# Kernel tuning notes

Measured on AMD Instinct MI355X. Metric: run time of the kernel, lower is better.

Reference implementation:

```python
import jax, jax.numpy as jnp
import numpy as np


def setup_inputs() -> dict:
    key = jax.random.key(0)
    k1, k2, k3 = jax.random.split(key, 3)
    B, C, E, L, W = 4, 2, 256, 16000, 40
    mixture_w = jax.random.normal(k1, (B, E, L), dtype=jnp.float32)
    est_mask = jax.random.uniform(k2, (B, C, E, L), dtype=jnp.float32)
    basis_w = jax.random.normal(k3, (W, E), dtype=jnp.float32) * (1.0 / np.sqrt(E))
    return {"mixture_w": mixture_w, "est_mask": est_mask, "basis_w": basis_w}


def overlap_and_add(frames, frame_step):
    # frames: [B, C, L, W] -> [B, C, T] with T = (L-1)*frame_step + W
    B, C, L, W = frames.shape
    T = (L - 1) * frame_step + W
    # scatter-add each frame into the output waveform at its strided offset
    idx = (jnp.arange(L)[:, None] * frame_step + jnp.arange(W)[None, :]).reshape(-1)
    out = jnp.zeros((B, C, T), dtype=frames.dtype)
    return out.at[..., idx].add(frames.reshape(B, C, L * W))


def reference(mixture_w, est_mask, basis_w):
    # mixture_w: [B, E, L], est_mask: [B, C, E, L], basis_w: [W, E]
    source_w = mixture_w[:, None, :, :] * est_mask          # [B, C, E, L]
    # transpose(2,3) then Linear(E->W): contract over E
    est_frames = jnp.einsum('bcel,we->bclw', source_w, basis_w)  # [B, C, L, W]
    W = basis_w.shape[0]
    return overlap_and_add(est_frames, W // 2)              # [B, C, T]
```

## Files before the change

### kernel.cpp

```cpp
#include <hip/hip_runtime.h>

#define BQ   4
#define CQ   2
#define EQ   256
#define LQ   16000
#define WQ   40
#define STEP 20
#define TQ   ((LQ - 1) * STEP + WQ)
#define TLF  255
#define OWN  (TLF * STEP)
#define NBX  63
#define SPAN (TLF * STEP + WQ)

__global__ void transpose_basis_kernel(const float* __restrict__ basis,
                                       float* __restrict__ wsT) {
    int i = blockIdx.x * 256 + threadIdx.x;
    if (i < EQ * WQ) {
        int e = i / WQ;
        int w = i - e * WQ;
        wsT[i] = basis[w * EQ + e];
    }
}

__global__ __launch_bounds__(256, 4) void decoder_kernel(
    const float* __restrict__ mix,
    const float* __restrict__ mask,
    const float* __restrict__ wsT,
    float* __restrict__ out)
{
    __shared__ float outS[SPAN];

    const int tid = threadIdx.x;
    const int ll  = tid;
    const int bx  = blockIdx.x;
    const int b   = blockIdx.y;
    const int c   = blockIdx.z;
    const int f   = TLF * bx - 1 + ll;

    const int   fc    = min(max(f, 0), LQ - 1);
    const float valid = (f >= 0 && f < LQ) ? 1.0f : 0.0f;

    float acc[WQ];
#pragma unroll
    for (int w = 0; w < WQ; ++w) acc[w] = 0.0f;

    const float* mp = mix  + (size_t)b * EQ * LQ + fc;
    const float* kp = mask + ((size_t)(b * CQ + c)) * EQ * LQ + fc;

    for (int eo = 0; eo < EQ; eo += 4) {
        float m[4], k[4];
#pragma unroll
        for (int u = 0; u < 4; ++u) {
            m[u] = mp[(size_t)(eo + u) * LQ];
            k[u] = kp[(size_t)(eo + u) * LQ];
        }
#pragma unroll
        for (int u = 0; u < 4; ++u) {
            const float s  = m[u] * k[u] * valid;
            const float* bb = wsT + (eo + u) * WQ;
#pragma unroll
            for (int w = 0; w < WQ; ++w) acc[w] = fmaf(s, bb[w], acc[w]);
        }
    }

    const int base = ll * STEP;
    if ((ll & 1) == 0) {
#pragma unroll
        for (int w = 0; w < WQ; ++w) outS[base + w] = acc[w];
    }
    __syncthreads();
    if (ll & 1) {
#pragma unroll
        for (int w = 0; w < WQ; ++w) outS[base + w] += acc[w];
    }
    __syncthreads();

    const size_t ob = ((size_t)b * CQ + c) * TQ + (size_t)OWN * bx;
    for (int i = tid; i < OWN; i += 256) {
        const long t = (long)OWN * bx + i;
        if (t < (long)TQ) {
            out[ob + i] = outS[STEP + i];
        }
    }
}

extern "C" void kernel_launch(void* const* d_in, const int* in_sizes, int n_in,
                              void* d_out, int out_size, void* d_ws, size_t ws_size,
                              hipStream_t stream) {
    const float* mix   = (const float*)d_in[0];
    const float* mask  = (const float*)d_in[1];
    const float* basis = (const float*)d_in[2];
    float* out = (float*)d_out;
    float* wsT = (float*)d_ws;

    transpose_basis_kernel<<<dim3((EQ * WQ + 255) / 256), 256, 0, stream>>>(basis, wsT);

    dim3 grid(NBX, BQ, CQ);
    decoder_kernel<<<grid, 256, 0, stream>>>(mix, mask, wsT, out);
}
```

Before: 283.4 us.

## Split E reduction across waves, stage basis in LDS, four frames per thread

Each of the four waves in a block now reduces over its own quarter of the E dimension instead of each thread walking all 256. Each lane accumulates four frames in float4 registers, and the basis is staged once into shared memory and read back as broadcast float4 values. The four per-wave partial results are combined through two shared overlap-add buffers in four serialized phases, and the two buffers are summed at write-out. The goal is more independent loads in flight and a shorter serial dependency chain per thread, at the cost of higher register use (launch bounds lowered to 2), larger LDS use and extra barriers.

```diff
diff --git a/kernel.cpp b/kernel.cpp
--- a/kernel.cpp
+++ b/kernel.cpp
@@ -11,6 +11,9 @@
 #define OWN  (TLF * STEP)
 #define NBX  63
 #define SPAN (TLF * STEP + WQ)
+#define NH   4
+#define EH   (EQ / NH)
+#define FPT  4
 
 __global__ void transpose_basis_kernel(const float* __restrict__ basis,
                                        float* __restrict__ wsT) {
@@ -22,56 +25,121 @@
     }
 }
 
-__global__ __launch_bounds__(256, 4) void decoder_kernel(
+__global__ __launch_bounds__(256, 2) void decoder_kernel(
     const float* __restrict__ mix,
     const float* __restrict__ mask,
     const float* __restrict__ wsT,
     float* __restrict__ out)
 {
-    __shared__ float outS[SPAN];
+    __shared__ __align__(16) float smem[2 * SPAN];
 
-    const int tid = threadIdx.x;
-    const int ll  = tid;
-    const int bx  = blockIdx.x;
-    const int b   = blockIdx.y;
-    const int c   = blockIdx.z;
-    const int f   = TLF * bx - 1 + ll;
+    const int tid  = threadIdx.x;
+    const int lane = tid & 63;
+    const int wv   = tid >> 6;
+    const int bx   = blockIdx.x;
+    const int b    = blockIdx.y;
+    const int c    = blockIdx.z;
 
-    const int   fc    = min(max(f, 0), LQ - 1);
-    const float valid = (f >= 0 && f < LQ) ? 1.0f : 0.0f;
+    float* basisT = smem;
+    for (int i = tid; i < EQ * WQ; i += 256) basisT[i] = wsT[i];
+    __syncthreads();
 
-    float acc[WQ];
+    int   fc[FPT];
+    float valid[FPT];
 #pragma unroll
-    for (int w = 0; w < WQ; ++w) acc[w] = 0.0f;
+    for (int j = 0; j < FPT; ++j) {
+        int f = TLF * bx - 1 + (j * 64 + lane);
+        fc[j]    = min(max(f, 0), LQ - 1);
+        valid[j] = (f >= 0 && f < LQ) ? 1.0f : 0.0f;
+    }
 
-    const float* mp = mix  + (size_t)b * EQ * LQ + fc;
-    const float* kp = mask + ((size_t)(b * CQ + c)) * EQ * LQ + fc;
+    float4 acc[FPT][WQ / 4];
+#pragma unroll
+    for (int j = 0; j < FPT; ++j)
+#pragma unroll
+        for (int t = 0; t < WQ / 4; ++t) acc[j][t] = make_float4(0.f, 0.f, 0.f, 0.f);
 
-    for (int eo = 0; eo < EQ; eo += 4) {
-        float m[4], k[4];
+    const size_t mb = ((size_t)b * EQ + wv * EH) * LQ;
+    const size_t kb = (((size_t)(b * CQ + c)) * EQ + wv * EH) * LQ;
+
+#pragma unroll 2
+    for (int e = 0; e < EH; ++e) {
+        float s[FPT];
 #pragma unroll
-        for (int u = 0; u < 4; ++u) {
-            m[u] = mp[(size_t)(eo + u) * LQ];
-            k[u] = kp[(size_t)(eo + u) * LQ];
+        for (int j = 0; j < FPT; ++j) {
+            float m = mix [mb + (size_t)e * LQ + fc[j]];
+            float k = mask[kb + (size_t)e * LQ + fc[j]];
+            s[j] = m * k * valid[j];
         }
+        const float4* bt = (const float4*)&basisT[(wv * EH + e) * WQ];
 #pragma unroll
-        for (int u = 0; u < 4; ++u) {
-            const float s  = m[u] * k[u] * valid;
-            const float* bb = wsT + (eo + u) * WQ;
+        for (int t = 0; t < WQ / 4; ++t) {
+            float4 bv = bt[t];
 #pragma unroll
-            for (int w = 0; w < WQ; ++w) acc[w] = fmaf(s, bb[w], acc[w]);
+            for (int j = 0; j < FPT; ++j) {
+                acc[j][t].x = fmaf(s[j], bv.x, acc[j][t].x);
+                acc[j][t].y = fmaf(s[j], bv.y, acc[j][t].y);
+                acc[j][t].z = fmaf(s[j], bv.z, acc[j][t].z);
+                acc[j][t].w = fmaf(s[j], bv.w, acc[j][t].w);
+            }
         }
     }
+    __syncthreads();
 
-    const int base = ll * STEP;
-    if ((ll & 1) == 0) {
+    float4* outC = (float4*)(smem + (wv >> 1) * SPAN);
+    const int hp = wv & 1;
+    const int lp = lane & 1;
+
+    if (hp == 0 && lp == 0) {
 #pragma unroll
-        for (int w = 0; w < WQ; ++w) outS[base + w] = acc[w];
+        for (int j = 0; j < FPT; ++j) {
+            float4* p = outC + (j * 64 + lane) * (STEP / 4) * 4 / 4;
+            p = (float4*)((float*)outC + (j * 64 + lane) * STEP);
+#pragma unroll
+            for (int t = 0; t < WQ / 4; ++t) p[t] = acc[j][t];
+        }
     }
     __syncthreads();
-    if (ll & 1) {
+    if (hp == 0 && lp == 1) {
 #pragma unroll
-        for (int w = 0; w < WQ; ++w) outS[base + w] += acc[w];
+        for (int j = 0; j < FPT; ++j) {
+            float4* p = (float4*)((float*)outC + (j * 64 + lane) * STEP);
+#pragma unroll
+            for (int t = 0; t < WQ / 4; ++t) {
+                float4 v = p[t];
+                v.x += acc[j][t].x; v.y += acc[j][t].y;
+                v.z += acc[j][t].z; v.w += acc[j][t].w;
+                p[t] = v;
+            }
+        }
+    }
+    __syncthreads();
+    if (hp == 1 && lp == 0) {
+#pragma unroll
+        for (int j = 0; j < FPT; ++j) {
+            float4* p = (float4*)((float*)outC + (j * 64 + lane) * STEP);
+#pragma unroll
+            for (int t = 0; t < WQ / 4; ++t) {
+                float4 v = p[t];
+                v.x += acc[j][t].x; v.y += acc[j][t].y;
+                v.z += acc[j][t].z; v.w += acc[j][t].w;
+                p[t] = v;
+            }
+        }
+    }
+    __syncthreads();
+    if (hp == 1 && lp == 1) {
+#pragma unroll
+        for (int j = 0; j < FPT; ++j) {
+            float4* p = (float4*)((float*)outC + (j * 64 + lane) * STEP);
+#pragma unroll
+            for (int t = 0; t < WQ / 4; ++t) {
+                float4 v = p[t];
+                v.x += acc[j][t].x; v.y += acc[j][t].y;
+                v.z += acc[j][t].z; v.w += acc[j][t].w;
+                p[t] = v;
+            }
+        }
     }
     __syncthreads();
 
@@ -79,7 +147,7 @@
     for (int i = tid; i < OWN; i += 256) {
         const long t = (long)OWN * bx + i;
         if (t < (long)TQ) {
-            out[ob + i] = outS[STEP + i];
+            out[ob + i] = smem[STEP + i] + smem[SPAN + STEP + i];
         }
     }
 }
```

Result: faster. 251.9 us (-11.1%).

## Split E across waves, register-block four frames per lane, stage basis in LDS

Applied to the files above, without the earlier changes.

The kernel is restructured so that each of the four waves reduces a quarter of the E dimension. Each lane loads float4 vectors of mix and mask covering four adjacent frames, with a two-deep software prefetch, and computes a 4x40 register tile against a basis transposed and staged in LDS. Partial frames are combined through LDS in four serialized phases, and the block tiling changes to 252 owned frames per block with a halo. The aim is to cut per-frame global load and basis-fetch overhead and raise arithmetic reuse. In exchange, 160 accumulators per thread raise register pressure and lower occupancy, and the reduction adds extra syncs.

```diff
diff --git a/kernel.cpp b/kernel.cpp
--- a/kernel.cpp
+++ b/kernel.cpp
@@ -7,10 +7,14 @@
 #define WQ   40
 #define STEP 20
 #define TQ   ((LQ - 1) * STEP + WQ)
-#define TLF  255
-#define OWN  (TLF * STEP)
-#define NBX  63
-#define SPAN (TLF * STEP + WQ)
+#define FBP  252
+#define NBX  64
+#define SPAN (255 * STEP + WQ)
+#define OWNP (FBP * STEP)
+#define OWNE (OWNP + STEP)
+#define NH   4
+#define EH   (EQ / NH)
+#define FPT  4
 
 __global__ void transpose_basis_kernel(const float* __restrict__ basis,
                                        float* __restrict__ wsT) {
@@ -22,64 +26,117 @@
     }
 }
 
-__global__ __launch_bounds__(256, 4) void decoder_kernel(
+__global__ __launch_bounds__(256) void decoder_kernel(
     const float* __restrict__ mix,
     const float* __restrict__ mask,
     const float* __restrict__ wsT,
     float* __restrict__ out)
 {
-    __shared__ float outS[SPAN];
+    __shared__ __align__(16) float smem[2 * SPAN];
 
-    const int tid = threadIdx.x;
-    const int ll  = tid;
-    const int bx  = blockIdx.x;
-    const int b   = blockIdx.y;
-    const int c   = blockIdx.z;
-    const int f   = TLF * bx - 1 + ll;
+    const int tid  = threadIdx.x;
+    const int lane = tid & 63;
+    const int wv   = tid >> 6;
+    const int bx   = blockIdx.x;
+    const int b    = blockIdx.y;
+    const int c    = blockIdx.z;
 
-    const int   fc    = min(max(f, 0), LQ - 1);
-    const float valid = (f >= 0 && f < LQ) ? 1.0f : 0.0f;
+    float* basisT = smem;
+    for (int i = tid; i < EQ * WQ; i += 256) basisT[i] = wsT[i];
+    __syncthreads();
 
-    float acc[WQ];
+    const int f0  = FBP * bx + FPT * lane;
+    const int f0c = min(f0, LQ - 4);
+    float4 valid;
+    valid.x = (f0 + 0 < LQ) ? 1.0f : 0.0f;
+    valid.y = (f0 + 1 < LQ) ? 1.0f : 0.0f;
+    valid.z = (f0 + 2 < LQ) ? 1.0f : 0.0f;
+    valid.w = (f0 + 3 < LQ) ? 1.0f : 0.0f;
+
+    float4 acc[FPT][WQ / 4];
 #pragma unroll
-    for (int w = 0; w < WQ; ++w) acc[w] = 0.0f;
+    for (int j = 0; j < FPT; ++j)
+#pragma unroll
+        for (int t = 0; t < WQ / 4; ++t) acc[j][t] = make_float4(0.f, 0.f, 0.f, 0.f);
 
-    const float* mp = mix  + (size_t)b * EQ * LQ + fc;
-    const float* kp = mask + ((size_t)(b * CQ + c)) * EQ * LQ + fc;
+    const float* mp = mix  + ((size_t)b * EQ + wv * EH) * LQ + f0c;
+    const float* kp = mask + (((size_t)(b * CQ + c)) * EQ + wv * EH) * LQ + f0c;
 
-    for (int eo = 0; eo < EQ; eo += 4) {
-        float m[4], k[4];
+    float4 mS[2], kS[2];
+    mS[0] = *(const float4*)(mp);
+    kS[0] = *(const float4*)(kp);
+    mS[1] = *(const float4*)(mp + LQ);
+    kS[1] = *(const float4*)(kp + LQ);
+
+    for (int eo = 0; eo < EH; eo += 2) {
 #pragma unroll
-        for (int u = 0; u < 4; ++u) {
-            m[u] = mp[(size_t)(eo + u) * LQ];
-            k[u] = kp[(size_t)(eo + u) * LQ];
+        for (int st = 0; st < 2; ++st) {
+            const int e = eo + st;
+            float4 s4;
+            s4.x = mS[st].x * kS[st].x * valid.x;
+            s4.y = mS[st].y * kS[st].y * valid.y;
+            s4.z = mS[st].z * kS[st].z * valid.z;
+            s4.w = mS[st].w * kS[st].w * valid.w;
+            const int en = min(e + 2, EH - 1);
+            mS[st] = *(const float4*)(mp + (size_t)en * LQ);
+            kS[st] = *(const float4*)(kp + (size_t)en * LQ);
+            const float4* bt = (const float4*)&basisT[(wv * EH + e) * WQ];
+#pragma unroll
+            for (int t = 0; t < WQ / 4; ++t) {
+                float4 bv = bt[t];
+                acc[0][t].x = fmaf(s4.x, bv.x, acc[0][t].x);
+                acc[0][t].y = fmaf(s4.x, bv.y, acc[0][t].y);
+                acc[0][t].z = fmaf(s4.x, bv.z, acc[0][t].z);
+                acc[0][t].w = fmaf(s4.x, bv.w, acc[0][t].w);
+                acc[1][t].x = fmaf(s4.y, bv.x, acc[1][t].x);
+                acc[1][t].y = fmaf(s4.y, bv.y, acc[1][t].y);
+                acc[1][t].z = fmaf(s4.y, bv.z, acc[1][t].z);
+                acc[1][t].w = fmaf(s4.y, bv.w, acc[1][t].w);
+                acc[2][t].x = fmaf(s4.z, bv.x, acc[2][t].x);
+                acc[2][t].y = fmaf(s4.z, bv.y, acc[2][t].y);
+                acc[2][t].z = fmaf(s4.z, bv.z, acc[2][t].z);
+                acc[2][t].w = fmaf(s4.z, bv.w, acc[2][t].w);
+                acc[3][t].x = fmaf(s4.w, bv.x, acc[3][t].x);
+                acc[3][t].y = fmaf(s4.w, bv.y, acc[3][t].y);
+                acc[3][t].z = fmaf(s4.w, bv.z, acc[3][t].z);
+                acc[3][t].w = fmaf(s4.w, bv.w, acc[3][t].w);
+            }
         }
-#pragma unroll
-        for (int u = 0; u < 4; ++u) {
-            const float s  = m[u] * k[u] * valid;
-            const float* bb = wsT + (eo + u) * WQ;
-#pragma unroll
-            for (int w = 0; w < WQ; ++w) acc[w] = fmaf(s, bb[w], acc[w]);
-        }
-    }
-
-    const int base = ll * STEP;
-    if ((ll & 1) == 0) {
-#pragma unroll
-        for (int w = 0; w < WQ; ++w) outS[base + w] = acc[w];
-    }
-    __syncthreads();
-    if (ll & 1) {
-#pragma unroll
-        for (int w = 0; w < WQ; ++w) outS[base + w] += acc[w];
     }
     __syncthreads();
 
-    const size_t ob = ((size_t)b * CQ + c) * TQ + (size_t)OWN * bx;
-    for (int i = tid; i < OWN; i += 256) {
-        const long t = (long)OWN * bx + i;
-        if (t < (long)TQ) {
-            out[ob + i] = outS[STEP + i];
+    for (int i = tid; i < 2 * SPAN; i += 256) smem[i] = 0.0f;
+    __syncthreads();
+
+    float* outC = smem + (wv >> 1) * SPAN;
+    const int hp = wv & 1;
+    const int lp = lane & 1;
+#pragma unroll
+    for (int ph = 0; ph < 4; ++ph) {
+        if (hp == (ph >> 1) && lp == (ph & 1)) {
+#pragma unroll
+            for (int j = 0; j < FPT; ++j) {
+                float4* p = (float4*)(outC + (FPT * lane + j) * STEP);
+#pragma unroll
+                for (int t = 0; t < WQ / 4; ++t) {
+                    float4 v = p[t];
+                    v.x += acc[j][t].x; v.y += acc[j][t].y;
+                    v.z += acc[j][t].z; v.w += acc[j][t].w;
+                    p[t] = v;
+                }
+            }
+        }
+        __syncthreads();
+    }
+
+    const int start = (bx == 0) ? 0 : STEP;
+    const size_t ob = ((size_t)(b * CQ + c)) * TQ + (size_t)OWNP * bx;
+    for (int i = tid; i < OWNE; i += 256) {
+        if (i >= start) {
+            const long t = (long)OWNP * bx + i;
+            if (t < (long)TQ) {
+                out[ob + i] = smem[i] + smem[SPAN + i];
+            }
         }
     }
 }
```

Measured after the change: 271.9 us. 1.04x faster.

## Use fp16 MFMA for the frame projection with smaller per-block frame tiles

Applied to the files above, without the earlier changes.

Replaces the per-thread scalar FMA accumulation over 40 basis outputs with 16x16x32 fp16 MFMA instructions. The basis is pre-packed into MFMA B-fragments in workspace and staged into shared memory. Each block now computes 63 frames across four waves, and overlap-add is done by summing two halves of neighbouring frames from a shared frame buffer. This removes the FP32 FMA bottleneck and register pressure, but rounds activations and weights to fp16, which adds precision risk. It also uses more, smaller blocks with 16-lane coalesced loads.

```diff
diff --git a/kernel.cpp b/kernel.cpp
--- a/kernel.cpp
+++ b/kernel.cpp
@@ -7,79 +7,107 @@
 #define WQ   40
 #define STEP 20
 #define TQ   ((LQ - 1) * STEP + WQ)
-#define TLF  255
-#define OWN  (TLF * STEP)
-#define NBX  63
-#define SPAN (TLF * STEP + WQ)
+#define NBX  254
+#define OWN  1260
+#define NKC  8
+#define NNT  3
+#define FR   64
+#define FSTR 52
+#define NBF  (NKC * NNT * 4 * 64)
 
-__global__ void transpose_basis_kernel(const float* __restrict__ basis,
-                                       float* __restrict__ wsT) {
+typedef _Float16 f16x8 __attribute__((ext_vector_type(8)));
+typedef float    f32x4 __attribute__((ext_vector_type(4)));
+
+__global__ void build_bfrag_kernel(const float* __restrict__ basis,
+                                   unsigned* __restrict__ wsF) {
     int i = blockIdx.x * 256 + threadIdx.x;
-    if (i < EQ * WQ) {
-        int e = i / WQ;
-        int w = i - e * WQ;
-        wsT[i] = basis[w * EQ + e];
-    }
+    if (i >= NBF) return;
+    int p    = i & 3;
+    int lane = (i >> 2) & 63;
+    int q    = i >> 8;
+    int nt   = q % NNT;
+    int kc   = q / NNT;
+    int n = nt * 16 + (lane & 15);
+    int k = kc * 32 + (lane >> 4) * 8 + 2 * p;
+    float lo = (n < WQ) ? basis[n * EQ + k]     : 0.0f;
+    float hi = (n < WQ) ? basis[n * EQ + k + 1] : 0.0f;
+    union { _Float16 h[2]; unsigned u; } cv;
+    cv.h[0] = (_Float16)lo;
+    cv.h[1] = (_Float16)hi;
+    wsF[i] = cv.u;
 }
 
-__global__ __launch_bounds__(256, 4) void decoder_kernel(
+__global__ __launch_bounds__(256) void decoder_kernel(
     const float* __restrict__ mix,
     const float* __restrict__ mask,
-    const float* __restrict__ wsT,
+    const unsigned* __restrict__ wsF,
     float* __restrict__ out)
 {
-    __shared__ float outS[SPAN];
+    __shared__ unsigned bfragS[NBF];
+    __shared__ float frameBuf[FR * FSTR];
 
-    const int tid = threadIdx.x;
-    const int ll  = tid;
-    const int bx  = blockIdx.x;
-    const int b   = blockIdx.y;
-    const int c   = blockIdx.z;
-    const int f   = TLF * bx - 1 + ll;
+    const int tid  = threadIdx.x;
+    const int lane = tid & 63;
+    const int wv   = tid >> 6;
+    const int bx   = blockIdx.x;
+    const int b    = blockIdx.y;
+    const int c    = blockIdx.z;
 
-    const int   fc    = min(max(f, 0), LQ - 1);
-    const float valid = (f >= 0 && f < LQ) ? 1.0f : 0.0f;
+    for (int i = tid; i < NBF; i += 256) bfragS[i] = wsF[i];
+    __syncthreads();
 
-    float acc[WQ];
+    const int m    = lane & 15;
+    const int quad = lane >> 4;
+    const int f    = 63 * bx - 1 + 16 * wv + m;
+    const int fc   = min(max(f, 0), LQ - 1);
+    const float vf = (f >= 0 && f < LQ) ? 1.0f : 0.0f;
+
+    const float* mp = mix  + (size_t)b * EQ * LQ
+                            + (size_t)(quad * 8) * LQ + fc;
+    const float* kp = mask + ((size_t)(b * CQ + c)) * EQ * LQ
+                            + (size_t)(quad * 8) * LQ + fc;
+
+    f32x4 acc[NNT];
 #pragma unroll
-    for (int w = 0; w < WQ; ++w) acc[w] = 0.0f;
+    for (int nt = 0; nt < NNT; ++nt) acc[nt] = (f32x4){0.f, 0.f, 0.f, 0.f};
 
-    const float* mp = mix  + (size_t)b * EQ * LQ + fc;
-    const float* kp = mask + ((size_t)(b * CQ + c)) * EQ * LQ + fc;
+#pragma unroll
+    for (int kc = 0; kc < NKC; ++kc) {
+        float sv[8];
+#pragma unroll
+        for (int j = 0; j < 8; ++j) {
+            float mv = mp[(size_t)(kc * 32 + j) * LQ];
+            float kv = kp[(size_t)(kc * 32 + j) * LQ];
+            sv[j] = mv * kv * vf;
+        }
+        f16x8 a;
+#pragma unroll
+        for (int j = 0; j < 8; ++j) a[j] = (_Float16)sv[j];
 
-    for (int eo = 0; eo < EQ; eo += 4) {
-        float m[4], k[4];
 #pragma unroll
-        for (int u = 0; u < 4; ++u) {
-            m[u] = mp[(size_t)(eo + u) * LQ];
-            k[u] = kp[(size_t)(eo + u) * LQ];
-        }
-#pragma unroll
-        for (int u = 0; u < 4; ++u) {
-            const float s  = m[u] * k[u] * valid;
-            const float* bb = wsT + (eo + u) * WQ;
-#pragma unroll
-            for (int w = 0; w < WQ; ++w) acc[w] = fmaf(s, bb[w], acc[w]);
+        for (int nt = 0; nt < NNT; ++nt) {
+            union { uint4 u; f16x8 v; } bb;
+            bb.u = ((const uint4*)bfragS)[(kc * NNT + nt) * 64 + lane];
+            acc[nt] = __builtin_amdgcn_mfma_f32_16x16x32_f16(a, bb.v, acc[nt],
+                                                             0, 0, 0);
         }
     }
 
-    const int base = ll * STEP;
-    if ((ll & 1) == 0) {
 #pragma unroll
-        for (int w = 0; w < WQ; ++w) outS[base + w] = acc[w];
-    }
-    __syncthreads();
-    if (ll & 1) {
+    for (int nt = 0; nt < NNT; ++nt)
 #pragma unroll
-        for (int w = 0; w < WQ; ++w) outS[base + w] += acc[w];
-    }
+        for (int r = 0; r < 4; ++r)
+            frameBuf[(16 * wv + quad * 4 + r) * FSTR + nt * 16 + m] = acc[nt][r];
     __syncthreads();
 
-    const size_t ob = ((size_t)b * CQ + c) * TQ + (size_t)OWN * bx;
+    const size_t ob = ((size_t)(b * CQ + c)) * TQ + (size_t)OWN * bx;
     for (int i = tid; i < OWN; i += 256) {
         const long t = (long)OWN * bx + i;
         if (t < (long)TQ) {
-            out[ob + i] = outS[STEP + i];
+            int q20 = i / 20;
+            int r20 = i - q20 * 20;
+            out[ob + i] = frameBuf[(q20 + 1) * FSTR + r20]
+                        + frameBuf[q20 * FSTR + r20 + STEP];
         }
     }
 }
@@ -91,10 +119,10 @@
     const float* mask  = (const float*)d_in[1];
     const float* basis = (const float*)d_in[2];
     float* out = (float*)d_out;
-    float* wsT = (float*)d_ws;
+    unsigned* wsF = (unsigned*)d_ws;
 
-    transpose_basis_kernel<<<dim3((EQ * WQ + 255) / 256), 256, 0, stream>>>(basis, wsT);
+    build_bfrag_kernel<<<dim3((NBF + 255) / 256), 256, 0, stream>>>(basis, wsF);
 
     dim3 grid(NBX, BQ, CQ);
-    decoder_kernel<<<grid, 256, 0, stream>>>(mix, mask, wsT, out);
+    decoder_kernel<<<grid, 256, 0, stream>>>(mix, mask, wsF, out);
 }
```

Result: faster. 247.9 us (-12.5%).
